# Performance work log

Hardware: AMD Instinct MI355X
Metric: run time of the kernel (lower is better)

Reference implementation:

```python
import jax, jax.numpy as jnp
import numpy as np


def setup_inputs() -> dict:
    key = jax.random.key(0)
    k1, k2 = jax.random.split(key)
    B, C, H, W = 16, 256, 96, 96
    x1 = jax.random.normal(k1, (B, C, H, W), dtype=jnp.float32)
    x2 = jax.random.normal(k2, (B, C, H, W), dtype=jnp.float32)
    return {"x1": x1, "x2": x2, "k": 1, "d": 4, "s1": 1, "s2": 1}


def reference(x1, x2, k, d, s1, s2):
    """FlowNet-style correlation cost volume (k=1 pointwise patch).

    out[b, i, y, x] = (1/(k*k*C)) * sum_c x1[b,c,y,x] * x2_pad[b,c,y+dy_i,x+dx_i]
    for displacements (dy, dx) in [-d, d] with stride s2 (x2 zero-padded by d).
    Output strided by s1 over spatial dims. Output channels = (2*d//s2 + 1)**2.
    """
    assert k == 1, "reference specialized to k=1 (pointwise correlation)"
    B, C, H, W = x1.shape
    norm = 1.0 / (k * k * C)
    # zero-pad x2 by max displacement d on each spatial side
    x2p = jnp.pad(x2, ((0, 0), (0, 0), (d, d), (d, d)))
    offsets = list(range(-d, d + 1, s2))  # displacement grid (fixed, small)
    outs = []
    for dy in offsets:
        for dx in offsets:
            shifted = x2p[:, :, d + dy:d + dy + H, d + dx:d + dx + W]  # [B,C,H,W]
            outs.append(jnp.einsum('bchw,bchw->bhw', x1, shifted) * norm)
    out = jnp.stack(outs, axis=1)  # [B, D*D, H, W]
    return out[:, :, ::s1, ::s1]
```

## Files before the change

### kernel.cpp

```cpp
#include <hip/hip_runtime.h>


namespace {
constexpr int Bsz = 16, Cch = 256, Hh = 96, Ww = 96;
constexpr int Dd = 4, NDisp = 9;
constexpr int TH = 4;
constexpr int PX = 8;
constexpr int NSTRIP = Ww / PX;
constexpr int CC = 4;
constexpr int X2ROWS = TH + 2 * Dd;
constexpr int X2P = 105;
constexpr int NT = TH * NDisp * NSTRIP;
constexpr int HW = Hh * Ww;
constexpr int X1_LDS = CC * TH * Ww;
constexpr int X2_LDS = CC * X2ROWS * X2P;
constexpr int X1_F4 = X1_LDS / 4;
constexpr int X2_GROUPS = 26;
constexpr int X2_F4 = CC * X2ROWS * X2_GROUPS;
constexpr int N_ITEMS = X1_F4 + X2_F4;
}

__global__ __launch_bounds__(NT, 2)
void corr81(const float* __restrict__ x1, const float* __restrict__ x2,
            float* __restrict__ out) {
  __shared__ float lds[X1_LDS + X2_LDS + 4];

  const int t = threadIdx.x;
  const int y0 = blockIdx.x * TH;
  const int b  = blockIdx.y;

  const int r   = t / (NDisp * NSTRIP);
  const int rem = t % (NDisp * NSTRIP);
  const int dyi = rem / NSTRIP;
  const int s   = rem % NSTRIP;
  const int x0  = s * PX;

  const float* __restrict__ x1b = x1 + (size_t)b * Cch * HW;
  const float* __restrict__ x2b = x2 + (size_t)b * Cch * HW;

  const float* gp[4];
  int  loff[4];
  bool zero[4];
#pragma unroll
  for (int j = 0; j < 4; ++j) {
    int i = t + j * NT;
    if (i >= N_ITEMS) {
      gp[j] = x1b; loff[j] = X1_LDS + X2_LDS; zero[j] = true;
    } else if (i < X1_F4) {
      int c = i / (TH * Ww / 4);
      int q = i % (TH * Ww / 4);
      gp[j]   = x1b + c * HW + y0 * Ww + q * 4;
      loff[j] = c * (TH * Ww) + q * 4;
      zero[j] = false;
    } else {
      int m  = i - X1_F4;
      int c  = m / (X2ROWS * X2_GROUPS);
      int m2 = m % (X2ROWS * X2_GROUPS);
      int ry = m2 / X2_GROUPS;
      int g  = m2 % X2_GROUPS;
      int gy = y0 + ry - Dd;
      bool z = (gy < 0) | (gy >= Hh) | (g == 0) | (g == X2_GROUPS - 1);
      gp[j]   = z ? x2b : (x2b + c * HW + gy * Ww + (g - 1) * 4);
      loff[j] = X1_LDS + c * (X2ROWS * X2P) + ry * X2P + g * 4;
      zero[j] = z;
    }
  }

  float acc[NDisp][PX];
#pragma unroll
  for (int i = 0; i < NDisp; ++i)
#pragma unroll
    for (int j = 0; j < PX; ++j) acc[i][j] = 0.f;

  float4 v[4];
#pragma unroll
  for (int j = 0; j < 4; ++j)
    v[j] = zero[j] ? make_float4(0.f, 0.f, 0.f, 0.f) : *(const float4*)gp[j];

  for (int c0 = 0; c0 < Cch; c0 += CC) {
    __syncthreads();
#pragma unroll
    for (int j = 0; j < 4; ++j) {
      int o = loff[j];
      if (o < X1_LDS) {
        *(float4*)(lds + o) = v[j];
      } else {
        lds[o] = v[j].x; lds[o + 1] = v[j].y; lds[o + 2] = v[j].z; lds[o + 3] = v[j].w;
      }
    }
    __syncthreads();
    if (c0 + CC < Cch) {
#pragma unroll
      for (int j = 0; j < 4; ++j) {
        gp[j] += CC * HW;
        v[j] = zero[j] ? make_float4(0.f, 0.f, 0.f, 0.f) : *(const float4*)gp[j];
      }
    }
#pragma unroll
    for (int cc = 0; cc < CC; ++cc) {
      const float* ap = lds + cc * (TH * Ww) + r * Ww + x0;
      float a[PX];
      *(float4*)(a)     = *(const float4*)(ap);
      *(float4*)(a + 4) = *(const float4*)(ap + 4);
      const float* bp = lds + X1_LDS + cc * (X2ROWS * X2P) + (r + dyi) * X2P + x0;
      float bb[PX + 2 * Dd];
#pragma unroll
      for (int q = 0; q < PX + 2 * Dd; ++q) bb[q] = bp[q];
#pragma unroll
      for (int dx = 0; dx < NDisp; ++dx)
#pragma unroll
        for (int px = 0; px < PX; ++px)
          acc[dx][px] += a[px] * bb[px + dx];
    }
  }

  const float nrm = 1.0f / (float)Cch;
  float* ob = out + ((size_t)b * (NDisp * NDisp) + (size_t)dyi * NDisp) * HW
                  + (size_t)(y0 + r) * Ww + x0;
#pragma unroll
  for (int dx = 0; dx < NDisp; ++dx) {
    float4 w0, w1;
    w0.x = acc[dx][0] * nrm; w0.y = acc[dx][1] * nrm;
    w0.z = acc[dx][2] * nrm; w0.w = acc[dx][3] * nrm;
    w1.x = acc[dx][4] * nrm; w1.y = acc[dx][5] * nrm;
    w1.z = acc[dx][6] * nrm; w1.w = acc[dx][7] * nrm;
    *(float4*)(ob + (size_t)dx * HW)     = w0;
    *(float4*)(ob + (size_t)dx * HW + 4) = w1;
  }
}

extern "C" void kernel_launch(void* const* d_in, const int* in_sizes, int n_in,
                              void* d_out, int out_size, void* d_ws, size_t ws_size,
                              hipStream_t stream) {
  const float* x1 = (const float*)d_in[0];
  const float* x2 = (const float*)d_in[1];
  float* out = (float*)d_out;
  dim3 grid(Hh / TH, Bsz);
  dim3 block(NT);
  hipLaunchKernelGGL(corr81, grid, block, 0, stream, x1, x2, out);
}
```

Measured before the change: 485.6 us.

## Split width into two tiles, vectorize padded x2 LDS access, raise occupancy

The image width is split into two 48-column tiles on a new grid dimension, so blocks shrink from 864 to 216 threads and the grid grows from 384 to 768 blocks. LDS rows are padded (52 and 60 floats) so the x2 halo tile is 16-byte aligned. That alignment allows float4 stores and float4 reads of the 16-wide x2 window in place of scalar accesses. Launch bounds request 3 blocks per CU, aiming at better occupancy and cheaper LDS traffic, at the cost of extra x2 halo reloads per tile.

```diff
diff --git a/kernel.cpp b/kernel.cpp
--- a/kernel.cpp
+++ b/kernel.cpp
@@ -2,38 +2,42 @@
 
 
 namespace {
-constexpr int Bsz = 16, Cch = 256, Hh = 96, Ww = 96;
-constexpr int Dd = 4, NDisp = 9;
+constexpr int Bsz = 16, Cch = 256, Hh = 96, Ww = 96, HW = Hh * Ww;
+constexpr int Dd = 4, ND = 9;
 constexpr int TH = 4;
+constexpr int TW = 48;
 constexpr int PX = 8;
-constexpr int NSTRIP = Ww / PX;
+constexpr int NS = TW / PX;
 constexpr int CC = 4;
-constexpr int X2ROWS = TH + 2 * Dd;
-constexpr int X2P = 105;
-constexpr int NT = TH * NDisp * NSTRIP;
-constexpr int HW = Hh * Ww;
-constexpr int X1_LDS = CC * TH * Ww;
-constexpr int X2_LDS = CC * X2ROWS * X2P;
-constexpr int X1_F4 = X1_LDS / 4;
-constexpr int X2_GROUPS = 26;
-constexpr int X2_F4 = CC * X2ROWS * X2_GROUPS;
-constexpr int N_ITEMS = X1_F4 + X2_F4;
+constexpr int NT = TH * ND * NS;
+constexpr int X2R = TH + 2 * Dd;
+constexpr int X1P = 52;
+constexpr int X2P = 60;
+constexpr int X1CH = TH * X1P;
+constexpr int X2CH = X2R * X2P;
+constexpr int X1SZ = CC * X1CH;
+constexpr int X2SZ = CC * X2CH;
+constexpr int X1G = TW / 4;
+constexpr int X2G = (TW + 2 * Dd) / 4;
+constexpr int N_X1 = CC * TH * X1G;
+constexpr int N_X2 = CC * X2R * X2G;
+constexpr int NI = N_X1 + N_X2;
 }
 
-__global__ __launch_bounds__(NT, 2)
+__global__ __launch_bounds__(NT, 3)
 void corr81(const float* __restrict__ x1, const float* __restrict__ x2,
             float* __restrict__ out) {
-  __shared__ float lds[X1_LDS + X2_LDS + 4];
+  __shared__ float lds[X1SZ + X2SZ];
 
-  const int t = threadIdx.x;
-  const int y0 = blockIdx.x * TH;
-  const int b  = blockIdx.y;
+  const int t   = threadIdx.x;
+  const int y0  = blockIdx.x * TH;
+  const int x0t = blockIdx.y * TW;
+  const int b   = blockIdx.z;
 
-  const int r   = t / (NDisp * NSTRIP);
-  const int rem = t % (NDisp * NSTRIP);
-  const int dyi = rem / NSTRIP;
-  const int s   = rem % NSTRIP;
-  const int x0  = s * PX;
+  const int r   = t / (ND * NS);
+  const int rem = t % (ND * NS);
+  const int dyi = rem / NS;
+  const int s   = rem % NS;
 
   const float* __restrict__ x1b = x1 + (size_t)b * Cch * HW;
   const float* __restrict__ x2b = x2 + (size_t)b * Cch * HW;
@@ -44,31 +48,30 @@
 #pragma unroll
   for (int j = 0; j < 4; ++j) {
     int i = t + j * NT;
-    if (i >= N_ITEMS) {
-      gp[j] = x1b; loff[j] = X1_LDS + X2_LDS; zero[j] = true;
-    } else if (i < X1_F4) {
-      int c = i / (TH * Ww / 4);
-      int q = i % (TH * Ww / 4);
-      gp[j]   = x1b + c * HW + y0 * Ww + q * 4;
-      loff[j] = c * (TH * Ww) + q * 4;
+    if (i < N_X1) {
+      int c  = i / (TH * X1G);
+      int rm = i % (TH * X1G);
+      int ry = rm / X1G, g = rm % X1G;
+      gp[j]   = x1b + c * HW + (y0 + ry) * Ww + x0t + 4 * g;
+      loff[j] = c * X1CH + ry * X1P + 4 * g;
       zero[j] = false;
     } else {
-      int m  = i - X1_F4;
-      int c  = m / (X2ROWS * X2_GROUPS);
-      int m2 = m % (X2ROWS * X2_GROUPS);
-      int ry = m2 / X2_GROUPS;
-      int g  = m2 % X2_GROUPS;
+      int m  = i - N_X1;
+      int c  = m / (X2R * X2G);
+      int rm = m % (X2R * X2G);
+      int ry = rm / X2G, g = rm % X2G;
       int gy = y0 + ry - Dd;
-      bool z = (gy < 0) | (gy >= Hh) | (g == 0) | (g == X2_GROUPS - 1);
-      gp[j]   = z ? x2b : (x2b + c * HW + gy * Ww + (g - 1) * 4);
-      loff[j] = X1_LDS + c * (X2ROWS * X2P) + ry * X2P + g * 4;
+      int gx = x0t + 4 * g - Dd;
+      bool z = (gy < 0) | (gy >= Hh) | (gx < 0) | (gx > Ww - 4);
+      gp[j]   = z ? x2b : (x2b + c * HW + gy * Ww + gx);
+      loff[j] = X1SZ + c * X2CH + ry * X2P + 4 * g;
       zero[j] = z;
     }
   }
 
-  float acc[NDisp][PX];
+  float acc[ND][PX];
 #pragma unroll
-  for (int i = 0; i < NDisp; ++i)
+  for (int i = 0; i < ND; ++i)
 #pragma unroll
     for (int j = 0; j < PX; ++j) acc[i][j] = 0.f;
 
@@ -80,14 +83,8 @@
   for (int c0 = 0; c0 < Cch; c0 += CC) {
     __syncthreads();
 #pragma unroll
-    for (int j = 0; j < 4; ++j) {
-      int o = loff[j];
-      if (o < X1_LDS) {
-        *(float4*)(lds + o) = v[j];
-      } else {
-        lds[o] = v[j].x; lds[o + 1] = v[j].y; lds[o + 2] = v[j].z; lds[o + 3] = v[j].w;
-      }
-    }
+    for (int j = 0; j < 4; ++j)
+      *(float4*)(lds + loff[j]) = v[j];
     __syncthreads();
     if (c0 + CC < Cch) {
 #pragma unroll
@@ -98,16 +95,17 @@
     }
 #pragma unroll
     for (int cc = 0; cc < CC; ++cc) {
-      const float* ap = lds + cc * (TH * Ww) + r * Ww + x0;
+      const float* ap = lds + cc * X1CH + r * X1P + PX * s;
       float a[PX];
       *(float4*)(a)     = *(const float4*)(ap);
       *(float4*)(a + 4) = *(const float4*)(ap + 4);
-      const float* bp = lds + X1_LDS + cc * (X2ROWS * X2P) + (r + dyi) * X2P + x0;
-      float bb[PX + 2 * Dd];
+      const float* bp = lds + X1SZ + cc * X2CH + (r + dyi) * X2P + PX * s;
+      float bb[16];
 #pragma unroll
-      for (int q = 0; q < PX + 2 * Dd; ++q) bb[q] = bp[q];
+      for (int q = 0; q < 4; ++q)
+        *(float4*)(bb + 4 * q) = *(const float4*)(bp + 4 * q);
 #pragma unroll
-      for (int dx = 0; dx < NDisp; ++dx)
+      for (int dx = 0; dx < ND; ++dx)
 #pragma unroll
         for (int px = 0; px < PX; ++px)
           acc[dx][px] += a[px] * bb[px + dx];
@@ -115,10 +113,10 @@
   }
 
   const float nrm = 1.0f / (float)Cch;
-  float* ob = out + ((size_t)b * (NDisp * NDisp) + (size_t)dyi * NDisp) * HW
-                  + (size_t)(y0 + r) * Ww + x0;
+  float* ob = out + ((size_t)b * (ND * ND) + (size_t)dyi * ND) * HW
+                  + (size_t)(y0 + r) * Ww + x0t + PX * s;
 #pragma unroll
-  for (int dx = 0; dx < NDisp; ++dx) {
+  for (int dx = 0; dx < ND; ++dx) {
     float4 w0, w1;
     w0.x = acc[dx][0] * nrm; w0.y = acc[dx][1] * nrm;
     w0.z = acc[dx][2] * nrm; w0.w = acc[dx][3] * nrm;
@@ -135,7 +133,7 @@
   const float* x1 = (const float*)d_in[0];
   const float* x2 = (const float*)d_in[1];
   float* out = (float*)d_out;
-  dim3 grid(Hh / TH, Bsz);
+  dim3 grid(Hh / TH, Ww / TW, Bsz);
   dim3 block(NT);
   hipLaunchKernelGGL(corr81, grid, block, 0, stream, x1, x2, out);
 }
```

After: 646.2 us. +33.1%, slower.
